# Performance work log

Measured on AMD Instinct MI355X. Metric: run time of the kernel, lower is better.

Reference implementation:

```python
import jax, jax.numpy as jnp
import numpy as np

ALPHA = 0.25
GAMMA = 2.0
EPS = 1e-4

B, A, C, M = 4, 100000, 80, 32


def setup_inputs() -> dict:
    key = jax.random.key(0)
    k1, k2, k3, k4, k5, k6 = jax.random.split(key, 6)
    clsfs = jax.random.uniform(k1, (B, A, C), dtype=jnp.float32)
    rgrss = jax.random.normal(k2, (B, A, 4), dtype=jnp.float32)
    # anchors: random centers/sizes on a 512x512 image, converted to x1y1x2y2
    ctr = jax.random.uniform(k3, (A, 2), minval=32.0, maxval=480.0)
    wh = jax.random.uniform(k4, (A, 2), minval=16.0, maxval=256.0)
    anc = jnp.concatenate([ctr - 0.5 * wh, ctr + 0.5 * wh], axis=1)
    ancs = anc[None, :, :].astype(jnp.float32)
    # annotations: [x1,y1,x2,y2,label]; all valid labels in [0, C)
    gctr = jax.random.uniform(k5, (B, M, 2), minval=64.0, maxval=448.0)
    gwh = jax.random.uniform(k6, (B, M, 2), minval=24.0, maxval=200.0)
    lbl = jax.random.randint(jax.random.fold_in(key, 7), (B, M, 1), 0, C).astype(jnp.float32)
    annos = jnp.concatenate([gctr - 0.5 * gwh, gctr + 0.5 * gwh, lbl], axis=2).astype(jnp.float32)
    return {"clsfs": clsfs, "rgrss": rgrss, "ancs": ancs, "annos": annos}


def calc_iou(a, b):
    # a: [A,4], b: [M,4] -> [A,M]
    area_b = (b[:, 2] - b[:, 0]) * (b[:, 3] - b[:, 1])
    area_a = (a[:, 2] - a[:, 0]) * (a[:, 3] - a[:, 1])
    iw = jnp.clip(jnp.minimum(a[:, None, 2], b[None, :, 2]) - jnp.maximum(a[:, None, 0], b[None, :, 0]), 0.0)
    ih = jnp.clip(jnp.minimum(a[:, None, 3], b[None, :, 3]) - jnp.maximum(a[:, None, 1], b[None, :, 1]), 0.0)
    inter = iw * ih
    ua = jnp.clip(area_a[:, None] + area_b[None, :] - inter, 1e-8)
    return inter / ua


def _per_image(clsf, rgrs, anns, anc, ancw, anch, ancx, ancy):
    valid = anns[:, 4] != -1.0  # [M]
    has_anns = valid.any()
    ious = calc_iou(anc, anns[:, :4])  # [A,M]
    ious = jnp.where(valid[None, :], ious, -1.0)  # mask padded annotations
    maxiou = ious.max(axis=1)
    maxidx = ious.argmax(axis=1)
    assigned = anns[maxidx]  # [A,5]
    pos = maxiou >= 0.5
    posnum = pos.sum().astype(clsf.dtype)

    # classification targets: -1 ignore, 0 negative (<0.4), one-hot for pos
    clsf = jnp.clip(clsf, EPS, 1.0 - EPS)
    nc = clsf.shape[1]
    targets = jnp.full(clsf.shape, -1.0, dtype=clsf.dtype)
    targets = jnp.where((maxiou < 0.4)[:, None], 0.0, targets)
    onehot = jnp.arange(nc)[None, :] == assigned[:, 4].astype(jnp.int32)[:, None]
    targets = jnp.where(pos[:, None], jnp.where(onehot, 1.0, 0.0), targets)

    alpha = jnp.where(targets == 1.0, ALPHA, 1.0 - ALPHA)
    focal = alpha * jnp.where(targets == 1.0, 1.0 - clsf, clsf) ** GAMMA
    bce = -(targets * jnp.log(clsf) + (1.0 - targets) * jnp.log(1.0 - clsf))
    clsloss = jnp.where(targets != -1.0, focal * bce, 0.0).sum() / jnp.maximum(posnum, 1.0)

    gtw0 = assigned[:, 2] - assigned[:, 0]
    gth0 = assigned[:, 3] - assigned[:, 1]
    gtx = assigned[:, 0] + 0.5 * gtw0
    gty = assigned[:, 1] + 0.5 * gth0
    gtw = jnp.maximum(gtw0, 1.0)
    gth = jnp.maximum(gth0, 1.0)
    t = jnp.stack([(gtx - ancx) / ancw,
                   (gty - ancy) / anch,
                   jnp.log(gtw / ancw),
                   jnp.log(gth / anch)], axis=1)
    t = t / jnp.array([0.1, 0.1, 0.2, 0.2], dtype=clsf.dtype)
    diff = jnp.abs(t - rgrs)
    sl1 = jnp.where(diff <= 1.0 / 9.0, 0.5 * 9.0 * diff * diff, diff - 0.5 / 9.0)
    regloss = jnp.where(pos[:, None], sl1, 0.0).sum() / jnp.maximum(posnum * 4.0, 1.0)
    regloss = jnp.where(posnum > 0, regloss, 0.0)

    clsloss = jnp.where(has_anns, clsloss, 0.0)
    regloss = jnp.where(has_anns, regloss, 0.0)
    return clsloss, regloss


def reference(clsfs, rgrss, ancs, annos):
    anc = ancs[0]
    ancw = anc[:, 2] - anc[:, 0]
    anch = anc[:, 3] - anc[:, 1]
    ancx = anc[:, 0] + 0.5 * ancw
    ancy = anc[:, 1] + 0.5 * anch
    cls_l, reg_l = jax.vmap(_per_image, in_axes=(0, 0, 0, None, None, None, None, None))(
        clsfs, rgrss, annos, anc, ancw, anch, ancx, ancy)
    return cls_l.mean(keepdims=True), reg_l.mean(keepdims=True)
```

## Files before the change

kernel.cpp:

```cpp
#include <hip/hip_runtime.h>

#define F_EPS 1e-4f

constexpr int B = 4, A = 100000, C = 80, M = 32;
constexpr int THREADS = 256;
constexpr int APB = 256;
constexpr int BPI = (A + APB - 1) / APB;
constexpr int VPA = C / 4;
constexpr int TVI = A * VPA;
constexpr int SBX = 512;
constexpr int SG = SBX * THREADS;
constexpr float WNEG = -0.5198603854199589f;

struct Part { float cls, reg, pos, pad; };

__global__ __launch_bounds__(THREADS) void focal_assign(
    const float* __restrict__ clsfs,
    const float* __restrict__ rgrss,
    const float* __restrict__ ancs,
    const float* __restrict__ annos,
    float* __restrict__ wn,
    Part* __restrict__ part) {
  const int b = blockIdx.x / BPI;
  const int a = (blockIdx.x - b * BPI) * APB + threadIdx.x;
  const int tid = threadIdx.x;

  __shared__ float s_ann[M * 5];
  __shared__ float s_red[3][THREADS / 64];
  if (tid < M * 5) s_ann[tid] = annos[b * M * 5 + tid];
  __syncthreads();

  float reg_acc = 0.0f, corr_acc = 0.0f, pos_acc = 0.0f;

  if (a < A) {
    float wv = 0.0f;
    const float4 anc = ((const float4*)ancs)[a];
    const float ax1 = anc.x, ay1 = anc.y, ax2 = anc.z, ay2 = anc.w;
    const float area_a = (ax2 - ax1) * (ay2 - ay1);
    float maxiou = -2.0f;
    int maxidx = 0;
    #pragma unroll
    for (int m = 0; m < M; ++m) {
      const float bx1 = s_ann[m * 5 + 0], by1 = s_ann[m * 5 + 1];
      const float bx2 = s_ann[m * 5 + 2], by2 = s_ann[m * 5 + 3];
      float iou = -1.0f;
      if (s_ann[m * 5 + 4] != -1.0f) {
        float iw = fmaxf(fminf(ax2, bx2) - fmaxf(ax1, bx1), 0.0f);
        float ih = fmaxf(fminf(ay2, by2) - fmaxf(ay1, by1), 0.0f);
        float inter = iw * ih;
        float area_b = (bx2 - bx1) * (by2 - by1);
        float ua = fmaxf(area_a + area_b - inter, 1e-8f);
        iou = inter / ua;
      }
      if (iou > maxiou) { maxiou = iou; maxidx = m; }
    }
    if (maxiou >= 0.5f) {
      const int lbl = (int)s_ann[maxidx * 5 + 4];
      pos_acc = 1.0f;
      wv = 1.0f;
      float p = clsfs[((size_t)b * A + a) * C + lbl];
      p = fminf(fmaxf(p, F_EPS), 1.0f - F_EPS);
      const float q = 1.0f - p;
      corr_acc = 0.25f * q * q * (-__logf(p)) - 0.75f * p * p * (-__logf(q));
      const float bx1 = s_ann[maxidx * 5 + 0], by1 = s_ann[maxidx * 5 + 1];
      const float bx2 = s_ann[maxidx * 5 + 2], by2 = s_ann[maxidx * 5 + 3];
      const float ancw = ax2 - ax1, anch = ay2 - ay1;
      const float ancx = ax1 + 0.5f * ancw, ancy = ay1 + 0.5f * anch;
      const float gtw0 = bx2 - bx1, gth0 = by2 - by1;
      const float gtx = bx1 + 0.5f * gtw0, gty = by1 + 0.5f * gth0;
      const float gtw = fmaxf(gtw0, 1.0f), gth = fmaxf(gth0, 1.0f);
      const float t0 = ((gtx - ancx) / ancw) / 0.1f;
      const float t1 = ((gty - ancy) / anch) / 0.1f;
      const float t2 = __logf(gtw / ancw) / 0.2f;
      const float t3 = __logf(gth / anch) / 0.2f;
      const float4 r = ((const float4*)rgrss)[(size_t)b * A + a];
      const float th = 1.0f / 9.0f, hh = 0.5f / 9.0f;
      float d;
      d = fabsf(t0 - r.x); reg_acc += (d <= th) ? 4.5f * d * d : d - hh;
      d = fabsf(t1 - r.y); reg_acc += (d <= th) ? 4.5f * d * d : d - hh;
      d = fabsf(t2 - r.z); reg_acc += (d <= th) ? 4.5f * d * d : d - hh;
      d = fabsf(t3 - r.w); reg_acc += (d <= th) ? 4.5f * d * d : d - hh;
    } else if (maxiou < 0.4f) {
      wv = 1.0f;
    }
    wn[(size_t)b * A + a] = wv * WNEG;
  }

  float cls_f = corr_acc, reg_f = reg_acc, pos_f = pos_acc;
  #pragma unroll
  for (int off = 32; off > 0; off >>= 1) {
    cls_f += __shfl_down(cls_f, off);
    reg_f += __shfl_down(reg_f, off);
    pos_f += __shfl_down(pos_f, off);
  }
  const int wave = tid >> 6, lane = tid & 63;
  if (lane == 0) { s_red[0][wave] = cls_f; s_red[1][wave] = reg_f; s_red[2][wave] = pos_f; }
  __syncthreads();
  if (tid == 0) {
    float bc = 0.f, br = 0.f, bp = 0.f;
    #pragma unroll
    for (int v = 0; v < THREADS / 64; ++v) { bc += s_red[0][v]; br += s_red[1][v]; bp += s_red[2][v]; }
    Part q; q.cls = bc; q.reg = br; q.pos = bp; q.pad = 0.f;
    part[blockIdx.x] = q;
  }
}

__device__ __forceinline__ float gterm(float p) {
  const float pc = fminf(fmaxf(p, F_EPS), 1.0f - F_EPS);
  return pc * pc * __log2f(1.0f - pc);
}
__device__ __forceinline__ float gquad(float4 v) {
  return (gterm(v.x) + gterm(v.y)) + (gterm(v.z) + gterm(v.w));
}

__global__ __launch_bounds__(THREADS) void focal_stream(
    const float* __restrict__ clsfs,
    const float* __restrict__ wn,
    float* __restrict__ part2) {
  const int b = blockIdx.y;
  const float4* __restrict__ base = (const float4*)(clsfs + (size_t)b * A * C);
  const float* __restrict__ w = wn + (size_t)b * A;
  const int i0 = blockIdx.x * THREADS + threadIdx.x;

  float a0 = 0.f, a1 = 0.f, a2 = 0.f, a3 = 0.f;

  {
    float4 v0 = base[i0];
    float4 v1 = base[i0 + 1 * SG];
    float4 v2 = base[i0 + 2 * SG];
    float4 v3 = base[i0 + 3 * SG];
    float4 v4 = base[i0 + 4 * SG];
    float4 v5 = base[i0 + 5 * SG];
    float4 v6 = base[i0 + 6 * SG];
    float4 v7 = base[i0 + 7 * SG];
    float w0 = w[(i0) / VPA];
    float w1 = w[(i0 + 1 * SG) / VPA];
    float w2 = w[(i0 + 2 * SG) / VPA];
    float w3 = w[(i0 + 3 * SG) / VPA];
    float w4 = w[(i0 + 4 * SG) / VPA];
    float w5 = w[(i0 + 5 * SG) / VPA];
    float w6 = w[(i0 + 6 * SG) / VPA];
    float w7 = w[(i0 + 7 * SG) / VPA];
    a0 += w0 * gquad(v0);
    a1 += w1 * gquad(v1);
    a2 += w2 * gquad(v2);
    a3 += w3 * gquad(v3);
    a0 += w4 * gquad(v4);
    a1 += w5 * gquad(v5);
    a2 += w6 * gquad(v6);
    a3 += w7 * gquad(v7);
  }
  {
    float4 v0 = base[i0 + 8 * SG];
    float4 v1 = base[i0 + 9 * SG];
    float4 v2 = base[i0 + 10 * SG];
    float4 v3 = base[i0 + 11 * SG];
    float4 v4 = base[i0 + 12 * SG];
    float4 v5 = base[i0 + 13 * SG];
    float4 v6 = base[i0 + 14 * SG];
    float w0 = w[(i0 + 8 * SG) / VPA];
    float w1 = w[(i0 + 9 * SG) / VPA];
    float w2 = w[(i0 + 10 * SG) / VPA];
    float w3 = w[(i0 + 11 * SG) / VPA];
    float w4 = w[(i0 + 12 * SG) / VPA];
    float w5 = w[(i0 + 13 * SG) / VPA];
    float w6 = w[(i0 + 14 * SG) / VPA];
    a0 += w0 * gquad(v0);
    a1 += w1 * gquad(v1);
    a2 += w2 * gquad(v2);
    a3 += w3 * gquad(v3);
    a0 += w4 * gquad(v4);
    a1 += w5 * gquad(v5);
    a2 += w6 * gquad(v6);
  }
  {
    const int i = i0 + 15 * SG;
    if (i < TVI) a3 += w[i / VPA] * gquad(base[i]);
  }

  float cls = (a0 + a1) + (a2 + a3);
  #pragma unroll
  for (int off = 32; off > 0; off >>= 1) cls += __shfl_down(cls, off);

  __shared__ float s_red[THREADS / 64];
  const int wave = threadIdx.x >> 6, lane = threadIdx.x & 63;
  if (lane == 0) s_red[wave] = cls;
  __syncthreads();
  if (threadIdx.x == 0) {
    float bc = 0.f;
    #pragma unroll
    for (int v = 0; v < THREADS / 64; ++v) bc += s_red[v];
    part2[b * SBX + blockIdx.x] = bc;
  }
}

__global__ __launch_bounds__(256) void focal_final(
    const float* __restrict__ annos,
    const Part* __restrict__ part,
    const float* __restrict__ part2,
    float* __restrict__ out) {
  const int tid = threadIdx.x;
  const int wv = tid >> 6, lane = tid & 63;
  __shared__ float s_cls[4], s_reg[4];

  double c = 0.0, r = 0.0;
  float p = 0.f;
  for (int j = lane; j < BPI; j += 64) {
    const Part q = part[wv * BPI + j];
    c += (double)q.cls; r += (double)q.reg; p += q.pos;
  }
  for (int j = lane; j < SBX; j += 64) c += (double)part2[wv * SBX + j];
  #pragma unroll
  for (int off = 32; off > 0; off >>= 1) {
    c += __shfl_down(c, off);
    r += __shfl_down(r, off);
    p += __shfl_down(p, off);
  }
  const bool valid = (lane < M) && (annos[(wv * M + lane) * 5 + 4] != -1.0f);
  const bool has = __any(valid);
  if (lane == 0) {
    const float pn = p;
    float cls = (float)(c / (double)fmaxf(pn, 1.0f));
    float reg = (pn > 0.f) ? (float)(r / ((double)pn * 4.0)) : 0.0f;
    if (!has) { cls = 0.f; reg = 0.f; }
    s_cls[wv] = cls; s_reg[wv] = reg;
  }
  __syncthreads();
  if (tid == 0) {
    out[0] = (s_cls[0] + s_cls[1] + s_cls[2] + s_cls[3]) * 0.25f;
    out[1] = (s_reg[0] + s_reg[1] + s_reg[2] + s_reg[3]) * 0.25f;
  }
}

extern "C" void kernel_launch(void* const* d_in, const int* in_sizes, int n_in,
                              void* d_out, int out_size, void* d_ws, size_t ws_size,
                              hipStream_t stream) {
  const float* clsfs = (const float*)d_in[0];
  const float* rgrss = (const float*)d_in[1];
  const float* ancs  = (const float*)d_in[2];
  const float* annos = (const float*)d_in[3];
  float* out = (float*)d_out;

  Part*  part  = (Part*)d_ws;
  float* part2 = (float*)((char*)d_ws + 32768);
  float* wn    = (float*)((char*)d_ws + 65536);

  focal_assign<<<dim3(B * BPI), dim3(THREADS), 0, stream>>>(
      clsfs, rgrss, ancs, annos, wn, part);
  focal_stream<<<dim3(SBX, B), dim3(THREADS), 0, stream>>>(clsfs, wn, part2);
  focal_final<<<1, 256, 0, stream>>>(annos, part, part2, out);
}
```

Baseline: 49.64 us.

## Sum negative focal term over all anchors and subtract ignored rows in assign

The stream kernel now sums the negative focal term over every element without a per-anchor weight, so the wn weight array and its gathered loads go away. The assign kernel subtracts the contribution of ignored anchors (IoU between 0.4 and 0.5) by re-reading their full class rows, and the final kernel combines the two sums. This removes a 1.6 MB write and read plus the integer divisions in the streaming loop. In exchange there is extra divergent row reading in the assign kernel, and the result now depends on a subtraction that can lose precision.

```diff
diff --git a/kernel.cpp b/kernel.cpp
--- a/kernel.cpp
+++ b/kernel.cpp
@@ -10,16 +10,22 @@
 constexpr int TVI = A * VPA;
 constexpr int SBX = 512;
 constexpr int SG = SBX * THREADS;
-constexpr float WNEG = -0.5198603854199589f;
 
 struct Part { float cls, reg, pos, pad; };
+
+__device__ __forceinline__ float fterm(float p) {
+  p = fminf(fmaxf(p, F_EPS), 1.0f - F_EPS);
+  return p * p * (-__logf(1.0f - p));
+}
+__device__ __forceinline__ float fquad(float4 v) {
+  return (fterm(v.x) + fterm(v.y)) + (fterm(v.z) + fterm(v.w));
+}
 
 __global__ __launch_bounds__(THREADS) void focal_assign(
     const float* __restrict__ clsfs,
     const float* __restrict__ rgrss,
     const float* __restrict__ ancs,
     const float* __restrict__ annos,
-    float* __restrict__ wn,
     Part* __restrict__ part) {
   const int b = blockIdx.x / BPI;
   const int a = (blockIdx.x - b * BPI) * APB + threadIdx.x;
@@ -33,7 +39,6 @@
   float reg_acc = 0.0f, corr_acc = 0.0f, pos_acc = 0.0f;
 
   if (a < A) {
-    float wv = 0.0f;
     const float4 anc = ((const float4*)ancs)[a];
     const float ax1 = anc.x, ay1 = anc.y, ax2 = anc.z, ay2 = anc.w;
     const float area_a = (ax2 - ax1) * (ay2 - ay1);
@@ -57,7 +62,6 @@
     if (maxiou >= 0.5f) {
       const int lbl = (int)s_ann[maxidx * 5 + 4];
       pos_acc = 1.0f;
-      wv = 1.0f;
       float p = clsfs[((size_t)b * A + a) * C + lbl];
       p = fminf(fmaxf(p, F_EPS), 1.0f - F_EPS);
       const float q = 1.0f - p;
@@ -80,10 +84,14 @@
       d = fabsf(t1 - r.y); reg_acc += (d <= th) ? 4.5f * d * d : d - hh;
       d = fabsf(t2 - r.z); reg_acc += (d <= th) ? 4.5f * d * d : d - hh;
       d = fabsf(t3 - r.w); reg_acc += (d <= th) ? 4.5f * d * d : d - hh;
-    } else if (maxiou < 0.4f) {
-      wv = 1.0f;
+    } else if (!(maxiou < 0.4f)) {
+      const float4* __restrict__ row =
+          (const float4*)(clsfs + ((size_t)b * A + a) * C);
+      float s = 0.0f;
+      #pragma unroll
+      for (int k = 0; k < VPA; ++k) s += fquad(row[k]);
+      corr_acc = -0.75f * s;
     }
-    wn[(size_t)b * A + a] = wv * WNEG;
   }
 
   float cls_f = corr_acc, reg_f = reg_acc, pos_f = pos_acc;
@@ -105,77 +113,52 @@
   }
 }
 
-__device__ __forceinline__ float gterm(float p) {
-  const float pc = fminf(fmaxf(p, F_EPS), 1.0f - F_EPS);
-  return pc * pc * __log2f(1.0f - pc);
-}
-__device__ __forceinline__ float gquad(float4 v) {
-  return (gterm(v.x) + gterm(v.y)) + (gterm(v.z) + gterm(v.w));
-}
-
 __global__ __launch_bounds__(THREADS) void focal_stream(
     const float* __restrict__ clsfs,
-    const float* __restrict__ wn,
     float* __restrict__ part2) {
   const int b = blockIdx.y;
   const float4* __restrict__ base = (const float4*)(clsfs + (size_t)b * A * C);
-  const float* __restrict__ w = wn + (size_t)b * A;
   const int i0 = blockIdx.x * THREADS + threadIdx.x;
 
   float a0 = 0.f, a1 = 0.f, a2 = 0.f, a3 = 0.f;
 
   {
-    float4 v0 = base[i0];
-    float4 v1 = base[i0 + 1 * SG];
-    float4 v2 = base[i0 + 2 * SG];
-    float4 v3 = base[i0 + 3 * SG];
-    float4 v4 = base[i0 + 4 * SG];
-    float4 v5 = base[i0 + 5 * SG];
-    float4 v6 = base[i0 + 6 * SG];
-    float4 v7 = base[i0 + 7 * SG];
-    float w0 = w[(i0) / VPA];
-    float w1 = w[(i0 + 1 * SG) / VPA];
-    float w2 = w[(i0 + 2 * SG) / VPA];
-    float w3 = w[(i0 + 3 * SG) / VPA];
-    float w4 = w[(i0 + 4 * SG) / VPA];
-    float w5 = w[(i0 + 5 * SG) / VPA];
-    float w6 = w[(i0 + 6 * SG) / VPA];
-    float w7 = w[(i0 + 7 * SG) / VPA];
-    a0 += w0 * gquad(v0);
-    a1 += w1 * gquad(v1);
-    a2 += w2 * gquad(v2);
-    a3 += w3 * gquad(v3);
-    a0 += w4 * gquad(v4);
-    a1 += w5 * gquad(v5);
-    a2 += w6 * gquad(v6);
-    a3 += w7 * gquad(v7);
+    const float4 v0 = base[i0];
+    const float4 v1 = base[i0 + 1 * SG];
+    const float4 v2 = base[i0 + 2 * SG];
+    const float4 v3 = base[i0 + 3 * SG];
+    const float4 v4 = base[i0 + 4 * SG];
+    const float4 v5 = base[i0 + 5 * SG];
+    const float4 v6 = base[i0 + 6 * SG];
+    const float4 v7 = base[i0 + 7 * SG];
+    a0 += fquad(v0);
+    a1 += fquad(v1);
+    a2 += fquad(v2);
+    a3 += fquad(v3);
+    a0 += fquad(v4);
+    a1 += fquad(v5);
+    a2 += fquad(v6);
+    a3 += fquad(v7);
   }
   {
-    float4 v0 = base[i0 + 8 * SG];
-    float4 v1 = base[i0 + 9 * SG];
-    float4 v2 = base[i0 + 10 * SG];
-    float4 v3 = base[i0 + 11 * SG];
-    float4 v4 = base[i0 + 12 * SG];
-    float4 v5 = base[i0 + 13 * SG];
-    float4 v6 = base[i0 + 14 * SG];
-    float w0 = w[(i0 + 8 * SG) / VPA];
-    float w1 = w[(i0 + 9 * SG) / VPA];
-    float w2 = w[(i0 + 10 * SG) / VPA];
-    float w3 = w[(i0 + 11 * SG) / VPA];
-    float w4 = w[(i0 + 12 * SG) / VPA];
-    float w5 = w[(i0 + 13 * SG) / VPA];
-    float w6 = w[(i0 + 14 * SG) / VPA];
-    a0 += w0 * gquad(v0);
-    a1 += w1 * gquad(v1);
-    a2 += w2 * gquad(v2);
-    a3 += w3 * gquad(v3);
-    a0 += w4 * gquad(v4);
-    a1 += w5 * gquad(v5);
-    a2 += w6 * gquad(v6);
+    const float4 v0 = base[i0 + 8 * SG];
+    const float4 v1 = base[i0 + 9 * SG];
+    const float4 v2 = base[i0 + 10 * SG];
+    const float4 v3 = base[i0 + 11 * SG];
+    const float4 v4 = base[i0 + 12 * SG];
+    const float4 v5 = base[i0 + 13 * SG];
+    const float4 v6 = base[i0 + 14 * SG];
+    a0 += fquad(v0);
+    a1 += fquad(v1);
+    a2 += fquad(v2);
+    a3 += fquad(v3);
+    a0 += fquad(v4);
+    a1 += fquad(v5);
+    a2 += fquad(v6);
   }
   {
     const int i = i0 + 15 * SG;
-    if (i < TVI) a3 += w[i / VPA] * gquad(base[i]);
+    if (i < TVI) a3 += fquad(base[i]);
   }
 
   float cls = (a0 + a1) + (a2 + a3);
@@ -203,24 +186,25 @@
   const int wv = tid >> 6, lane = tid & 63;
   __shared__ float s_cls[4], s_reg[4];
 
-  double c = 0.0, r = 0.0;
+  double c = 0.0, r = 0.0, s = 0.0;
   float p = 0.f;
   for (int j = lane; j < BPI; j += 64) {
     const Part q = part[wv * BPI + j];
     c += (double)q.cls; r += (double)q.reg; p += q.pos;
   }
-  for (int j = lane; j < SBX; j += 64) c += (double)part2[wv * SBX + j];
+  for (int j = lane; j < SBX; j += 64) s += (double)part2[wv * SBX + j];
   #pragma unroll
   for (int off = 32; off > 0; off >>= 1) {
     c += __shfl_down(c, off);
     r += __shfl_down(r, off);
+    s += __shfl_down(s, off);
     p += __shfl_down(p, off);
   }
   const bool valid = (lane < M) && (annos[(wv * M + lane) * 5 + 4] != -1.0f);
   const bool has = __any(valid);
   if (lane == 0) {
     const float pn = p;
-    float cls = (float)(c / (double)fmaxf(pn, 1.0f));
+    float cls = (float)((0.75 * s + c) / (double)fmaxf(pn, 1.0f));
     float reg = (pn > 0.f) ? (float)(r / ((double)pn * 4.0)) : 0.0f;
     if (!has) { cls = 0.f; reg = 0.f; }
     s_cls[wv] = cls; s_reg[wv] = reg;
@@ -243,10 +227,9 @@
 
   Part*  part  = (Part*)d_ws;
   float* part2 = (float*)((char*)d_ws + 32768);
-  float* wn    = (float*)((char*)d_ws + 65536);
 
   focal_assign<<<dim3(B * BPI), dim3(THREADS), 0, stream>>>(
-      clsfs, rgrss, ancs, annos, wn, part);
-  focal_stream<<<dim3(SBX, B), dim3(THREADS), 0, stream>>>(clsfs, wn, part2);
+      clsfs, rgrss, ancs, annos, part);
+  focal_stream<<<dim3(SBX, B), dim3(THREADS), 0, stream>>>(clsfs, part2);
   focal_final<<<1, 256, 0, stream>>>(annos, part, part2, out);
 }
```

Measured after the change: 68.01 us. +37.0%, slower.
